# Kernel optimization log

Measured on AMD Instinct MI355X. Metric: run time of the kernel, lower is better.

## Reference

```python
import jax, jax.numpy as jnp
import numpy as np

N = 50000
E = 1600000
NEG_SLOPE = 0.2
BN_EPS = 1e-5


def gat_conv(x, src, dst, W, a_s, a_d, b):
    """PyG-style GATConv (concat=True). a_s/a_d: [H, C]."""
    H, C = a_s.shape
    h = (x @ W).reshape(-1, H, C)  # [N, H, C]
    alpha_src = jnp.einsum('nhc,hc->nh', h, a_s)  # [N, H]
    alpha_dst = jnp.einsum('nhc,hc->nh', h, a_d)  # [N, H]
    e = jax.nn.leaky_relu(alpha_src[src] + alpha_dst[dst], NEG_SLOPE)  # [E, H]
    # segment softmax over edges sharing the same destination node
    m = jax.ops.segment_max(e, dst, num_segments=N)
    e = jnp.exp(e - m[dst])
    s = jax.ops.segment_sum(e, dst, num_segments=N)
    alpha = e / (s[dst] + 1e-16)  # [E, H]
    msg = h[src] * alpha[:, :, None]  # [E, H, C]
    out = jax.ops.segment_sum(msg, dst, num_segments=N)  # [N, H, C]
    return out.reshape(-1, H * C) + b


def batch_norm(x, g, beta):
    mu = jnp.mean(x, axis=0)
    var = jnp.var(x, axis=0)
    return (x - mu) * jax.lax.rsqrt(var + BN_EPS) * g + beta


def setup_inputs() -> dict:
    key = jax.random.key(0)
    ks = jax.random.split(key, 20)
    d_in, hid, heads, d_out = 128, 16, 4, 40
    hh = hid * heads  # 64
    inp = {
        'x': jax.random.normal(ks[0], (N, d_in), jnp.float32),
        'edge_index': jax.random.randint(ks[1], (2, E), 0, N, jnp.int32),
        # layer 0: in -> hid*heads
        'W0': jax.random.normal(ks[2], (d_in, hh), jnp.float32) * 0.05,
        'a_src0': jax.random.normal(ks[3], (heads, hid), jnp.float32) * 0.05,
        'a_dst0': jax.random.normal(ks[4], (heads, hid), jnp.float32) * 0.05,
        'b0': jnp.zeros((hh,), jnp.float32),
        'g0': jnp.ones((hh,), jnp.float32),
        'beta0': jnp.zeros((hh,), jnp.float32),
        # layer 1: hid*heads -> hid*heads
        'W1': jax.random.normal(ks[5], (hh, hh), jnp.float32) * 0.1,
        'a_src1': jax.random.normal(ks[6], (heads, hid), jnp.float32) * 0.1,
        'a_dst1': jax.random.normal(ks[7], (heads, hid), jnp.float32) * 0.1,
        'b1': jnp.zeros((hh,), jnp.float32),
        'g1': jnp.ones((hh,), jnp.float32),
        'beta1': jnp.zeros((hh,), jnp.float32),
        # layer 2: hid*heads -> out, heads=1
        'W2': jax.random.normal(ks[8], (hh, d_out), jnp.float32) * 0.1,
        'a_src2': jax.random.normal(ks[9], (1, d_out), jnp.float32) * 0.1,
        'a_dst2': jax.random.normal(ks[10], (1, d_out), jnp.float32) * 0.1,
        'b2': jnp.zeros((d_out,), jnp.float32),
    }
    return inp


def reference(x, edge_index, W0, a_src0, a_dst0, b0, g0, beta0,
              W1, a_src1, a_dst1, b1, g1, beta1,
              W2, a_src2, a_dst2, b2):
    # add self-loops (PyG GATConv default)
    loop = jnp.arange(N, dtype=edge_index.dtype)
    src = jnp.concatenate([edge_index[0], loop])
    dst = jnp.concatenate([edge_index[1], loop])

    h = gat_conv(x, src, dst, W0, a_src0, a_dst0, b0)
    h = jax.nn.relu(batch_norm(h, g0, beta0))
    h = gat_conv(h, src, dst, W1, a_src1, a_dst1, b1)
    h = jax.nn.relu(batch_norm(h, g1, beta1))
    h = gat_conv(h, src, dst, W2, a_src2, a_dst2, b2)
    return jax.nn.log_softmax(h, axis=-1)
```

## Files before the change

### kernel.cpp

```cpp
#include <hip/hip_runtime.h>
#include <math.h>

#define NEG_SLOPE 0.2f
#define CAP 128
#define BCAP 6144

__device__ __forceinline__ unsigned enc_f(float f) {
    unsigned b = __float_as_uint(f);
    return (b & 0x80000000u) ? ~b : (b | 0x80000000u);
}
__device__ __forceinline__ float dec_f(unsigned u) {
    return (u & 0x80000000u) ? __uint_as_float(u ^ 0x80000000u) : __uint_as_float(~u);
}
#define ENC_NEG_INF 0x007FFFFFu

__device__ __forceinline__ unsigned short f2bf(float f) {
    unsigned u = __float_as_uint(f);
    u += 0x7fffu + ((u >> 16) & 1u);
    return (unsigned short)(u >> 16);
}
__device__ __forceinline__ float bf2f(unsigned short b) {
    return __uint_as_float(((unsigned)b) << 16);
}

static inline int nblk(long total, int b) { return (int)((total + b - 1) / b); }

__global__ void init_kernel(int* bincnt, float* bn, unsigned* menc, int nbin) {
    int i = blockIdx.x * blockDim.x + threadIdx.x;
    if (i < nbin) bincnt[i] = 0;
    if (i < 256) bn[i] = 0.f;
    if (i < 16) menc[i] = ENC_NEG_INF;
}

__global__ void bin_kernel(const int* __restrict__ srcs, const int* __restrict__ dsts,
                           int E_, int EA, int nbin, int* bincnt, unsigned* __restrict__ binbuf) {
    __shared__ int lh[512];
    __shared__ int lbase[512];
    int tid = threadIdx.x;
    for (int i = tid; i < nbin; i += 256) lh[i] = 0;
    __syncthreads();
    int chunk = (EA + gridDim.x - 1) / gridDim.x;
    int e0 = blockIdx.x * chunk;
    int e1 = e0 + chunk; if (e1 > EA) e1 = EA;
    for (int i = e0 + tid; i < e1; i += 256) {
        int d = (i < E_) ? dsts[i] : (i - E_);
        atomicAdd(&lh[d >> 7], 1);
    }
    __syncthreads();
    for (int i = tid; i < nbin; i += 256) {
        lbase[i] = atomicAdd(&bincnt[i], lh[i]);
        lh[i] = 0;
    }
    __syncthreads();
    for (int i = e0 + tid; i < e1; i += 256) {
        int s, d;
        if (i < E_) { s = srcs[i]; d = dsts[i]; } else { s = d = i - E_; }
        int b = d >> 7;
        int pos = lbase[b] + atomicAdd(&lh[b], 1);
        if (pos < BCAP) binbuf[(size_t)b * BCAP + pos] = ((unsigned)s << 16) | (unsigned)d;
    }
}

__global__ void build_kernel(const unsigned* __restrict__ binbuf, const int* __restrict__ bincnt,
                             unsigned short* __restrict__ esrc, int* __restrict__ cnt, int n) {
    __shared__ unsigned short slab[128 * CAP];
    __shared__ int lcnt[128];
    int tid = threadIdx.x;
    int b = blockIdx.x, d0 = b << 7;
    if (tid < 128) lcnt[tid] = 0;
    __syncthreads();
    int nb = bincnt[b]; if (nb > BCAP) nb = BCAP;
    for (int i = tid; i < nb; i += 256) {
        unsigned u = binbuf[(size_t)b * BCAP + i];
        int s = (int)(u >> 16);
        int ld = (int)(u & 0xffffu) - d0;
        int pos = atomicAdd(&lcnt[ld], 1);
        if (pos < CAP) slab[ld * CAP + pos] = (unsigned short)s;
    }
    __syncthreads();
    const uint4* sl = (const uint4*)slab;
    uint4* outp = (uint4*)esrc;
    for (int i = tid; i < 128 * CAP / 8; i += 256) {
        int r = i >> 4;
        if (d0 + r < n) outp[(size_t)(d0 + r) * (CAP / 8) + (i & 15)] = sl[i];
    }
    if (tid < 128 && d0 + tid < n) cnt[d0 + tid] = lcnt[tid];
}

template <int K, bool BN>
__global__ __launch_bounds__(256) void gemm_alpha_kernel(
    const float* __restrict__ X, const float* __restrict__ W,
    const float* __restrict__ a_s, const float* __restrict__ a_d,
    unsigned short* __restrict__ Hout, float* __restrict__ as_o,
    float* __restrict__ ad_o, unsigned* menc_, int n,
    const float* __restrict__ bnsum, const float* __restrict__ bnsq,
    const float* __restrict__ g, const float* __restrict__ beta) {
    __shared__ float Xs[32][132];
    __shared__ float Ws[32][64];
    __shared__ float scale[BN ? K : 4];
    __shared__ float shift[BN ? K : 4];
    __shared__ float redm[4][4];

    int tid = threadIdx.x;
    if (BN) {
        if (tid < K) {
            float inv_n = 1.0f / (float)n;
            float mu = bnsum[tid] * inv_n;
            float var = bnsq[tid] * inv_n - mu * mu;
            float sc = rsqrtf(var + 1e-5f) * g[tid];
            scale[tid] = sc;
            shift[tid] = beta[tid] - mu * sc;
        }
        __syncthreads();
    }

    int node0 = blockIdx.x * 128;
    int tx = tid & 7;
    int ty = tid >> 3;

    int snode = tid & 127;
    int khalf = (tid >> 7) * 16;
    int src_row = node0 + snode; if (src_row >= n) src_row = n - 1;
    const float* xrow = X + (size_t)src_row * K;

    float acc[4][8];
#pragma unroll
    for (int i = 0; i < 4; ++i)
#pragma unroll
        for (int j = 0; j < 8; ++j) acc[i][j] = 0.f;

    constexpr int NCH = K / 32;
    for (int c = 0; c < NCH; ++c) {
        int k0 = c * 32;
#pragma unroll
        for (int r = 0; r < 2; ++r) {
            int f = tid + r * 256;
            int kk = f >> 4;
            int cq = f & 15;
            float4 wv4 = *(const float4*)(W + (size_t)(k0 + kk) * 64 + cq * 4);
            *(float4*)&Ws[kk][cq * 4] = wv4;
        }
#pragma unroll
        for (int q = 0; q < 4; ++q) {
            int kk = khalf + q * 4;
            float4 v = *(const float4*)(xrow + k0 + kk);
            if (BN) {
                float4 sc = *(const float4*)(&scale[k0 + kk]);
                float4 sh = *(const float4*)(&shift[k0 + kk]);
                v.x = fmaxf(fmaf(v.x, sc.x, sh.x), 0.f);
                v.y = fmaxf(fmaf(v.y, sc.y, sh.y), 0.f);
                v.z = fmaxf(fmaf(v.z, sc.z, sh.z), 0.f);
                v.w = fmaxf(fmaf(v.w, sc.w, sh.w), 0.f);
            }
            Xs[kk + 0][snode] = v.x;
            Xs[kk + 1][snode] = v.y;
            Xs[kk + 2][snode] = v.z;
            Xs[kk + 3][snode] = v.w;
        }
        __syncthreads();
#pragma unroll 2
        for (int kk = 0; kk < 32; ++kk) {
            float4 xv = *(const float4*)(&Xs[kk][ty * 4]);
            float4 wa = *(const float4*)(&Ws[kk][tx * 8]);
            float4 wb = *(const float4*)(&Ws[kk][tx * 8 + 4]);
            float xs_[4] = {xv.x, xv.y, xv.z, xv.w};
            float ws_[8] = {wa.x, wa.y, wa.z, wa.w, wb.x, wb.y, wb.z, wb.w};
#pragma unroll
            for (int i = 0; i < 4; ++i)
#pragma unroll
                for (int j = 0; j < 8; ++j)
                    acc[i][j] = fmaf(xs_[i], ws_[j], acc[i][j]);
        }
        __syncthreads();
    }

    float4 asa = *(const float4*)(a_s + tx * 8);
    float4 asb = *(const float4*)(a_s + tx * 8 + 4);
    float4 ada = *(const float4*)(a_d + tx * 8);
    float4 adb = *(const float4*)(a_d + tx * 8 + 4);
    int head = tx >> 1;
    float p1v[4], p2v[4];
#pragma unroll
    for (int i = 0; i < 4; ++i) {
        float p1 = acc[i][0] * asa.x + acc[i][1] * asa.y + acc[i][2] * asa.z + acc[i][3] * asa.w
                 + acc[i][4] * asb.x + acc[i][5] * asb.y + acc[i][6] * asb.z + acc[i][7] * asb.w;
        float p2 = acc[i][0] * ada.x + acc[i][1] * ada.y + acc[i][2] * ada.z + acc[i][3] * ada.w
                 + acc[i][4] * adb.x + acc[i][5] * adb.y + acc[i][6] * adb.z + acc[i][7] * adb.w;
        p1 += __shfl_xor(p1, 1, 64);
        p2 += __shfl_xor(p2, 1, 64);
        p1v[i] = p1; p2v[i] = p2;
    }
#pragma unroll
    for (int i = 0; i < 4; ++i) {
        int node = node0 + ty * 4 + i;
        if (node < n) {
            unsigned r0 = (unsigned)f2bf(acc[i][0]) | ((unsigned)f2bf(acc[i][1]) << 16);
            unsigned r1 = (unsigned)f2bf(acc[i][2]) | ((unsigned)f2bf(acc[i][3]) << 16);
            unsigned r2 = (unsigned)f2bf(acc[i][4]) | ((unsigned)f2bf(acc[i][5]) << 16);
            unsigned r3 = (unsigned)f2bf(acc[i][6]) | ((unsigned)f2bf(acc[i][7]) << 16);
            *(uint4*)(Hout + (size_t)node * 64 + tx * 8) = make_uint4(r0, r1, r2, r3);
            if ((tx & 1) == 0) {
                as_o[(size_t)node * 4 + head] = p1v[i];
                ad_o[(size_t)node * 4 + head] = p2v[i];
            }
        }
    }
    float am = -1e30f;
    if ((tx & 1) == 0)
        am = fmaxf(fmaxf(p1v[0], p1v[1]), fmaxf(p1v[2], p1v[3]));
    am = fmaxf(am, __shfl_xor(am, 8, 64));
    am = fmaxf(am, __shfl_xor(am, 16, 64));
    am = fmaxf(am, __shfl_xor(am, 32, 64));
    int lane = tid & 63;
    if (lane < 8 && (lane & 1) == 0) redm[tid >> 6][lane >> 1] = am;
    __syncthreads();
    if (tid < 4) {
        float m = fmaxf(fmaxf(redm[0][tid], redm[1][tid]), fmaxf(redm[2][tid], redm[3][tid]));
        atomicMax(&menc_[tid], enc_f(m));
    }
}

__global__ void gather64_kernel(const int* __restrict__ cnt,
                                const unsigned short* __restrict__ esrc,
                                const float* __restrict__ as_, const float* __restrict__ ad_,
                                const unsigned short* __restrict__ Hf,
                                const unsigned* __restrict__ menc,
                                const float* __restrict__ bias, float* __restrict__ feat, int n) {
    int tid = threadIdx.x;
    int wv = tid >> 6, lane = tid & 63;
    int slot = lane >> 4, ql = lane & 15, hq = ql >> 2;
    int node = blockIdx.x * 4 + wv;
    if (node >= n) return;

    int deg = cnt[node]; if (deg > CAP) deg = CAP;
    const unsigned short* ep = esrc + (size_t)node * CAP;
    float4 adv = *(const float4*)(ad_ + (size_t)node * 4);
    float adh = (slot == 0) ? adv.x : (slot == 1) ? adv.y : (slot == 2) ? adv.z : adv.w;
    float mm = dec_f(menc[slot]) + adh;
    float mh = mm > 0.f ? mm : NEG_SLOPE * mm;

    float4 acc = make_float4(0.f, 0.f, 0.f, 0.f);
    float wp = 0.f;
    int nch = (deg + 15) >> 4;

    int lim0 = deg < 16 ? deg : 16;
    int s0 = (ql < lim0) ? (int)ep[ql] : 0;
    float aA = as_[(unsigned)(s0 * 4 + slot)];
    int sA = 0;
    if (nch > 1) {
        int l1 = deg - 16; if (l1 > 16) l1 = 16;
        sA = (ql < l1) ? (int)ep[16 + ql] : 0;
    }
    ushort4 hva[4], hvb[4];
#pragma unroll
    for (int i = 0; i < 4; ++i) {
        if (i * 4 >= lim0) break;
        int sj = __shfl(s0, i * 4 + slot, 64);
        hva[i] = *(const ushort4*)(Hf + (unsigned)(sj * 64 + ql * 4));
    }
    int sB = 0; float aB = 0.f;

#define G64_CHUNK(c, hC, hN, sC, sN, aC, aN)                                      \
    {                                                                             \
        int lim = deg - (c) * 16; if (lim > 16) lim = 16;                         \
        float ev = aC + adh;                                                      \
        ev = ev > 0.f ? ev : NEG_SLOPE * ev;                                      \
        float w = (ql < lim) ? __expf(ev - mh) : 0.f;                             \
        if ((c) + 1 < nch) aN = as_[(unsigned)(sC * 4 + slot)];                   \
        if ((c) + 2 < nch) {                                                      \
            int l2 = deg - ((c) + 2) * 16; if (l2 > 16) l2 = 16;                  \
            sN = (ql < l2) ? (int)ep[((c) + 2) * 16 + ql] : 0;                    \
        }                                                                         \
        if ((c) + 1 < nch) {                                                      \
            int limN = deg - ((c) + 1) * 16; if (limN > 16) limN = 16;            \
            _Pragma("unroll")                                                     \
            for (int i = 0; i < 4; ++i) {                                         \
                if (i * 4 >= limN) break;                                         \
                int sj = __shfl(sC, i * 4 + slot, 64);                            \
                hN[i] = *(const ushort4*)(Hf + (unsigned)(sj * 64 + ql * 4));     \
            }                                                                     \
        }                                                                         \
        wp += w;                                                                  \
        _Pragma("unroll")                                                         \
        for (int i = 0; i < 4; ++i) {                                             \
            if (i * 4 >= lim) break;                                              \
            int cj = i * 4 + slot;                                                \
            float wj = __shfl(w, hq * 16 + cj, 64);                               \
            ushort4 hv = hC[i];                                                   \
            acc.x = fmaf(bf2f(hv.x), wj, acc.x);                                  \
            acc.y = fmaf(bf2f(hv.y), wj, acc.y);                                  \
            acc.z = fmaf(bf2f(hv.z), wj, acc.z);                                  \
            acc.w = fmaf(bf2f(hv.w), wj, acc.w);                                  \
        }                                                                         \
    }

    for (int c = 0; c < nch; c += 2) {
        G64_CHUNK(c, hva, hvb, sA, sB, aA, aB);
        if (c + 1 < nch) G64_CHUNK(c + 1, hvb, hva, sB, sA, aB, aA);
    }
#undef G64_CHUNK

#pragma unroll
    for (int o = 16; o < 64; o <<= 1) {
        acc.x += __shfl_xor(acc.x, o, 64);
        acc.y += __shfl_xor(acc.y, o, 64);
        acc.z += __shfl_xor(acc.z, o, 64);
        acc.w += __shfl_xor(acc.w, o, 64);
    }
#pragma unroll
    for (int o = 1; o < 16; o <<= 1) wp += __shfl_xor(wp, o, 64);
    float wsh = __shfl(wp, hq << 4, 64);
    if (slot == 0) {
        float inv = 1.0f / (wsh + 1e-16f);
        float4 bv = *(const float4*)(bias + ql * 4);
        float4 rr;
        rr.x = fmaf(acc.x, inv, bv.x);
        rr.y = fmaf(acc.y, inv, bv.y);
        rr.z = fmaf(acc.z, inv, bv.z);
        rr.w = fmaf(acc.w, inv, bv.w);
        *(float4*)(feat + (size_t)node * 64 + ql * 4) = rr;
    }
}

__global__ void prep2_kernel(const float* __restrict__ feat, const float* __restrict__ bnsum,
                             const float* __restrict__ bnsq, const float* __restrict__ g,
                             const float* __restrict__ beta, const float* __restrict__ W2,
                             const float* __restrict__ as2v, const float* __restrict__ ad2v,
                             unsigned short* __restrict__ z, float* __restrict__ as_o,
                             float* __restrict__ ad_o, unsigned* menc_, int n) {
    __shared__ float sc[64], sh[64], vs[64], vd[64];
    int tid = threadIdx.x;
    if (tid < 64) {
        float inv_n = 1.0f / (float)n;
        float mu = bnsum[tid] * inv_n;
        float var = bnsq[tid] * inv_n - mu * mu;
        float s = rsqrtf(var + 1e-5f) * g[tid];
        sc[tid] = s;
        sh[tid] = beta[tid] - mu * s;
    } else if (tid < 128) {
        int k = tid - 64;
        float s1 = 0.f, s2 = 0.f;
        for (int j = 0; j < 40; ++j) {
            float wv = W2[k * 40 + j];
            s1 = fmaf(wv, as2v[j], s1);
            s2 = fmaf(wv, ad2v[j], s2);
        }
        vs[k] = s1;
        vd[k] = s2;
    }
    __syncthreads();
    int lane = tid & 63, wv = tid >> 6;
    float scl = sc[lane], shl = sh[lane], vsl = vs[lane], vdl = vd[lane];
    float amax = -1e30f;
    int nwaves = gridDim.x * 4;
    for (int node = blockIdx.x * 4 + wv; node < n; node += nwaves) {
        float v = fmaf(feat[(size_t)node * 64 + lane], scl, shl);
        v = v > 0.f ? v : 0.f;
        z[(size_t)node * 64 + lane] = f2bf(v);
        float p1 = v * vsl, p2 = v * vdl;
#pragma unroll
        for (int o = 1; o < 64; o <<= 1) {
            p1 += __shfl_xor(p1, o, 64);
            p2 += __shfl_xor(p2, o, 64);
        }
        amax = fmaxf(amax, p1);
        if (lane == 0) { as_o[node] = p1; ad_o[node] = p2; }
    }
    if (lane == 0) atomicMax(menc_, enc_f(amax));
}

__global__ void gatherz_kernel(const int* __restrict__ cnt,
                               const unsigned short* __restrict__ esrc,
                               const float* __restrict__ as_, const float* __restrict__ ad_,
                               const unsigned short* __restrict__ Z,
                               const unsigned* __restrict__ menc,
                               float* __restrict__ agg, int n) {
    int tid = threadIdx.x;
    int wv = tid >> 6, lane = tid & 63;
    int slot = lane >> 4, ql = lane & 15;
    int node = blockIdx.x * 4 + wv;
    if (node >= n) return;

    int deg = cnt[node]; if (deg > CAP) deg = CAP;
    const unsigned short* ep = esrc + (size_t)node * CAP;
    float adv = ad_[node];
    float mm = dec_f(menc[0]) + adv;
    float mh = mm > 0.f ? mm : NEG_SLOPE * mm;

    float4 acc = make_float4(0.f, 0.f, 0.f, 0.f);
    float wp = 0.f;
    for (int base = 0; base < deg; base += 64) {
        int lim = deg - base; if (lim > 64) lim = 64;
        int s = 0;
        if (lane < lim) s = (int)ep[base + lane];
        float asv = (lane < lim) ? as_[(unsigned)s] : 0.f;
        ushort4 hv[16];
#pragma unroll
        for (int i = 0; i < 16; ++i) {
            if (i * 4 >= lim) break;
            int sj = __shfl(s, i * 4 + slot, 64);
            hv[i] = *(const ushort4*)(Z + (unsigned)(sj * 64 + ql * 4));
        }
        float w = 0.f;
        if (lane < lim) {
            float ev = asv + adv;
            ev = ev > 0.f ? ev : NEG_SLOPE * ev;
            w = __expf(ev - mh);
        }
        wp += w;
#pragma unroll
        for (int i = 0; i < 16; ++i) {
            if (i * 4 >= lim) break;
            int cj = i * 4 + slot;
            float wj = __shfl(w, cj, 64);
            ushort4 h4 = hv[i];
            acc.x = fmaf(bf2f(h4.x), wj, acc.x);
            acc.y = fmaf(bf2f(h4.y), wj, acc.y);
            acc.z = fmaf(bf2f(h4.z), wj, acc.z);
            acc.w = fmaf(bf2f(h4.w), wj, acc.w);
        }
    }
#pragma unroll
    for (int o = 16; o < 64; o <<= 1) {
        acc.x += __shfl_xor(acc.x, o, 64);
        acc.y += __shfl_xor(acc.y, o, 64);
        acc.z += __shfl_xor(acc.z, o, 64);
        acc.w += __shfl_xor(acc.w, o, 64);
    }
#pragma unroll
    for (int o = 1; o < 64; o <<= 1) wp += __shfl_xor(wp, o, 64);
    if (slot == 0) {
        float inv = 1.0f / (wp + 1e-16f);
        float4 rr;
        rr.x = acc.x * inv;
        rr.y = acc.y * inv;
        rr.z = acc.z * inv;
        rr.w = acc.w * inv;
        *(float4*)(agg + (size_t)node * 64 + ql * 4) = rr;
    }
}

__global__ __launch_bounds__(256) void gemm_lsm_kernel(const float* __restrict__ X,
                                                       const float* __restrict__ W,
                                                       const float* __restrict__ bias,
                                                       float* __restrict__ out, int n) {
    __shared__ float Xs[32][132];
    __shared__ float Ws[32][40];
    __shared__ float bs[40];
    int tid = threadIdx.x;
    if (tid < 40) bs[tid] = bias[tid];

    int node0 = blockIdx.x * 128;
    int tx = tid & 7;
    int ty = tid >> 3;
    int snode = tid & 127;
    int khalf = (tid >> 7) * 16;
    int src_row = node0 + snode; if (src_row >= n) src_row = n - 1;
    const float* xrow = X + (size_t)src_row * 64;

    float acc[4][5];
#pragma unroll
    for (int i = 0; i < 4; ++i)
#pragma unroll
        for (int j = 0; j < 5; ++j) acc[i][j] = 0.f;

    for (int c = 0; c < 2; ++c) {
        int k0 = c * 32;
        for (int f = tid; f < 320; f += 256) {
            int kk = f / 10, q = f - kk * 10;
            *(float4*)&Ws[kk][q * 4] = *(const float4*)(W + (size_t)(k0 + kk) * 40 + q * 4);
        }
#pragma unroll
        for (int q = 0; q < 4; ++q) {
            int kk = khalf + q * 4;
            float4 v = *(const float4*)(xrow + k0 + kk);
            Xs[kk + 0][snode] = v.x;
            Xs[kk + 1][snode] = v.y;
            Xs[kk + 2][snode] = v.z;
            Xs[kk + 3][snode] = v.w;
        }
        __syncthreads();
#pragma unroll 2
        for (int kk = 0; kk < 32; ++kk) {
            float4 xv = *(const float4*)(&Xs[kk][ty * 4]);
            float w0 = Ws[kk][tx * 5 + 0];
            float w1 = Ws[kk][tx * 5 + 1];
            float w2 = Ws[kk][tx * 5 + 2];
            float w3 = Ws[kk][tx * 5 + 3];
            float w4 = Ws[kk][tx * 5 + 4];
            float xs_[4] = {xv.x, xv.y, xv.z, xv.w};
#pragma unroll
            for (int i = 0; i < 4; ++i) {
                acc[i][0] = fmaf(xs_[i], w0, acc[i][0]);
                acc[i][1] = fmaf(xs_[i], w1, acc[i][1]);
                acc[i][2] = fmaf(xs_[i], w2, acc[i][2]);
                acc[i][3] = fmaf(xs_[i], w3, acc[i][3]);
                acc[i][4] = fmaf(xs_[i], w4, acc[i][4]);
            }
        }
        __syncthreads();
    }

    float b0 = bs[tx * 5 + 0], b1 = bs[tx * 5 + 1], b2 = bs[tx * 5 + 2],
          b3 = bs[tx * 5 + 3], b4 = bs[tx * 5 + 4];
#pragma unroll
    for (int i = 0; i < 4; ++i) {
        float v0 = acc[i][0] + b0, v1 = acc[i][1] + b1, v2 = acc[i][2] + b2,
              v3 = acc[i][3] + b3, v4 = acc[i][4] + b4;
        float m = fmaxf(fmaxf(fmaxf(v0, v1), fmaxf(v2, v3)), v4);
        m = fmaxf(m, __shfl_xor(m, 1, 64));
        m = fmaxf(m, __shfl_xor(m, 2, 64));
        m = fmaxf(m, __shfl_xor(m, 4, 64));
        float ex = __expf(v0 - m) + __expf(v1 - m) + __expf(v2 - m)
                 + __expf(v3 - m) + __expf(v4 - m);
        ex += __shfl_xor(ex, 1, 64);
        ex += __shfl_xor(ex, 2, 64);
        ex += __shfl_xor(ex, 4, 64);
        float ls = m + logf(ex);
        int node = node0 + ty * 4 + i;
        if (node < n) {
            float* op = out + (size_t)node * 40 + tx * 5;
            op[0] = v0 - ls;
            op[1] = v1 - ls;
            op[2] = v2 - ls;
            op[3] = v3 - ls;
            op[4] = v4 - ls;
        }
    }
}

__global__ void bn_stats_kernel(const float* __restrict__ feat, float* bnsum, float* bnsq,
                                int n) {
    __shared__ float ls[256], lq[256];
    int f = threadIdx.x & 63, y = threadIdx.x >> 6;
    float ps = 0.f, pq = 0.f;
    for (int node = blockIdx.x * 4 + y; node < n; node += gridDim.x * 4) {
        float v = feat[(size_t)node * 64 + f];
        ps += v;
        pq += v * v;
    }
    ls[threadIdx.x] = ps;
    lq[threadIdx.x] = pq;
    __syncthreads();
    if (y == 0) {
        atomicAdd(&bnsum[f], ls[f] + ls[f + 64] + ls[f + 128] + ls[f + 192]);
        atomicAdd(&bnsq[f], lq[f] + lq[f + 64] + lq[f + 128] + lq[f + 192]);
    }
}

extern "C" void kernel_launch(void* const* d_in, const int* in_sizes, int n_in,
                              void* d_out, int out_size, void* d_ws, size_t ws_size,
                              hipStream_t stream) {
    const float* x   = (const float*)d_in[0];
    const int*   ei  = (const int*)d_in[1];
    const float* W0  = (const float*)d_in[2];
    const float* as0 = (const float*)d_in[3];
    const float* ad0 = (const float*)d_in[4];
    const float* b0  = (const float*)d_in[5];
    const float* g0  = (const float*)d_in[6];
    const float* be0 = (const float*)d_in[7];
    const float* W1  = (const float*)d_in[8];
    const float* as1 = (const float*)d_in[9];
    const float* ad1 = (const float*)d_in[10];
    const float* b1  = (const float*)d_in[11];
    const float* g1  = (const float*)d_in[12];
    const float* be1 = (const float*)d_in[13];
    const float* W2  = (const float*)d_in[14];
    const float* as2 = (const float*)d_in[15];
    const float* ad2 = (const float*)d_in[16];
    const float* b2  = (const float*)d_in[17];

    const int N  = in_sizes[0] / 128;
    const int E  = in_sizes[1] / 2;
    const int EA = E + N;
    const int NBIN = (N + 127) >> 7;
    const int* srcs = ei;
    const int* dsts = ei + E;

    float* ws    = (float*)d_ws;
    float* feat  = ws;
    float* agg   = feat + (size_t)N * 64;
    float* asrc  = agg + (size_t)N * 64;
    float* adst  = asrc + (size_t)N * 4;
    float* bn    = adst + (size_t)N * 4;
    unsigned* menc = (unsigned*)(bn + 256);
    int* bincnt  = (int*)(menc + 16);
    int* cnt     = bincnt + 512;
    unsigned short* hb   = (unsigned short*)(cnt + N);
    unsigned short* esrc = hb + (size_t)N * 64;
    unsigned* binbuf = (unsigned*)(esrc + (size_t)N * CAP);

    float* bn0sum = bn, *bn0sq = bn + 64, *bn1sum = bn + 128, *bn1sq = bn + 192;

    init_kernel<<<2, 256, 0, stream>>>(bincnt, bn, menc, NBIN);
    bin_kernel<<<512, 256, 0, stream>>>(srcs, dsts, E, EA, NBIN, bincnt, binbuf);
    build_kernel<<<NBIN, 256, 0, stream>>>(binbuf, bincnt, esrc, cnt, N);

    gemm_alpha_kernel<128, false><<<nblk(N, 128), 256, 0, stream>>>(
        x, W0, as0, ad0, hb, asrc, adst, menc, N, nullptr, nullptr, nullptr, nullptr);
    gather64_kernel<<<nblk(N, 4), 256, 0, stream>>>(cnt, esrc, asrc, adst, hb, menc, b0, feat, N);
    bn_stats_kernel<<<512, 256, 0, stream>>>(feat, bn0sum, bn0sq, N);

    gemm_alpha_kernel<64, true><<<nblk(N, 128), 256, 0, stream>>>(
        feat, W1, as1, ad1, hb, asrc, adst, menc + 4, N, bn0sum, bn0sq, g0, be0);
    gather64_kernel<<<nblk(N, 4), 256, 0, stream>>>(cnt, esrc, asrc, adst, hb, menc + 4, b1,
                                                    feat, N);
    bn_stats_kernel<<<512, 256, 0, stream>>>(feat, bn1sum, bn1sq, N);

    prep2_kernel<<<512, 256, 0, stream>>>(feat, bn1sum, bn1sq, g1, be1, W2, as2, ad2,
                                          hb, asrc, adst, menc + 8, N);
    gatherz_kernel<<<nblk(N, 4), 256, 0, stream>>>(cnt, esrc, asrc, adst, hb, menc + 8, agg, N);
    gemm_lsm_kernel<<<nblk(N, 128), 256, 0, stream>>>(agg, W2, b2, (float*)d_out, N);
}
```

Baseline: 368.3 us.

## Deepen gather prefetch to three-stage rotating buffers in 64-wide GAT aggregation

Changes the per-node edge aggregation loop from double-buffered to triple-buffered prefetch, so neighbor feature rows are loaded two chunks ahead instead of one. It also drops the per-iteration early-break guards in the gather and FMA loops, loading padded entries from index 0 and multiplying them by zero weights. The aim is to hide more gather latency. The cost is more registers, which may lower occupancy, and some wasted loads on partial chunks.

```diff
diff --git a/kernel.cpp b/kernel.cpp
--- a/kernel.cpp
+++ b/kernel.cpp
@@ -243,62 +243,73 @@
     float wp = 0.f;
     int nch = (deg + 15) >> 4;
 
-    int lim0 = deg < 16 ? deg : 16;
-    int s0 = (ql < lim0) ? (int)ep[ql] : 0;
-    float aA = as_[(unsigned)(s0 * 4 + slot)];
+    ushort4 h0[4], h1[4], h2[4];
+    int l0 = deg < 16 ? deg : 16;
+    int sP0 = (ql < l0) ? (int)ep[ql] : 0;
+    float aA = as_[(unsigned)(sP0 * 4 + slot)];
     int sA = 0;
     if (nch > 1) {
         int l1 = deg - 16; if (l1 > 16) l1 = 16;
         sA = (ql < l1) ? (int)ep[16 + ql] : 0;
     }
-    ushort4 hva[4], hvb[4];
+    int sB = 0;
+    if (nch > 2) {
+        int l2 = deg - 32; if (l2 > 16) l2 = 16;
+        sB = (ql < l2) ? (int)ep[32 + ql] : 0;
+    }
 #pragma unroll
     for (int i = 0; i < 4; ++i) {
-        if (i * 4 >= lim0) break;
-        int sj = __shfl(s0, i * 4 + slot, 64);
-        hva[i] = *(const ushort4*)(Hf + (unsigned)(sj * 64 + ql * 4));
-    }
-    int sB = 0; float aB = 0.f;
-
-#define G64_CHUNK(c, hC, hN, sC, sN, aC, aN)                                      \
-    {                                                                             \
-        int lim = deg - (c) * 16; if (lim > 16) lim = 16;                         \
-        float ev = aC + adh;                                                      \
-        ev = ev > 0.f ? ev : NEG_SLOPE * ev;                                      \
-        float w = (ql < lim) ? __expf(ev - mh) : 0.f;                             \
-        if ((c) + 1 < nch) aN = as_[(unsigned)(sC * 4 + slot)];                   \
-        if ((c) + 2 < nch) {                                                      \
-            int l2 = deg - ((c) + 2) * 16; if (l2 > 16) l2 = 16;                  \
-            sN = (ql < l2) ? (int)ep[((c) + 2) * 16 + ql] : 0;                    \
-        }                                                                         \
-        if ((c) + 1 < nch) {                                                      \
-            int limN = deg - ((c) + 1) * 16; if (limN > 16) limN = 16;            \
-            _Pragma("unroll")                                                     \
-            for (int i = 0; i < 4; ++i) {                                         \
-                if (i * 4 >= limN) break;                                         \
-                int sj = __shfl(sC, i * 4 + slot, 64);                            \
-                hN[i] = *(const ushort4*)(Hf + (unsigned)(sj * 64 + ql * 4));     \
-            }                                                                     \
-        }                                                                         \
-        wp += w;                                                                  \
-        _Pragma("unroll")                                                         \
-        for (int i = 0; i < 4; ++i) {                                             \
-            if (i * 4 >= lim) break;                                              \
-            int cj = i * 4 + slot;                                                \
-            float wj = __shfl(w, hq * 16 + cj, 64);                               \
-            ushort4 hv = hC[i];                                                   \
-            acc.x = fmaf(bf2f(hv.x), wj, acc.x);                                  \
-            acc.y = fmaf(bf2f(hv.y), wj, acc.y);                                  \
-            acc.z = fmaf(bf2f(hv.z), wj, acc.z);                                  \
-            acc.w = fmaf(bf2f(hv.w), wj, acc.w);                                  \
-        }                                                                         \
-    }
-
-    for (int c = 0; c < nch; c += 2) {
-        G64_CHUNK(c, hva, hvb, sA, sB, aA, aB);
-        if (c + 1 < nch) G64_CHUNK(c + 1, hvb, hva, sB, sA, aB, aA);
-    }
-#undef G64_CHUNK
+        int sj = __shfl(sP0, i * 4 + slot, 64);
+        h0[i] = *(const ushort4*)(Hf + (unsigned)(sj * 64 + ql * 4));
+    }
+    float aB = 0.f;
+    if (nch > 1) {
+        aB = as_[(unsigned)(sA * 4 + slot)];
+#pragma unroll
+        for (int i = 0; i < 4; ++i) {
+            int sj = __shfl(sA, i * 4 + slot, 64);
+            h1[i] = *(const ushort4*)(Hf + (unsigned)(sj * 64 + ql * 4));
+        }
+    }
+    float aC = 0.f;
+    int sC = 0;
+
+#define GBODY(cc, HC, HD, S2, S3, AC, A2)                                     \
+    {                                                                         \
+        int lim = deg - (cc) * 16; if (lim > 16) lim = 16;                    \
+        float ev = AC + adh;                                                  \
+        ev = ev > 0.f ? ev : NEG_SLOPE * ev;                                  \
+        float w = (ql < lim) ? __expf(ev - mh) : 0.f;                         \
+        if ((cc) + 2 < nch) A2 = as_[(unsigned)(S2 * 4 + slot)];              \
+        if ((cc) + 3 < nch) {                                                 \
+            int l3 = deg - ((cc) + 3) * 16; if (l3 > 16) l3 = 16;             \
+            S3 = (ql < l3) ? (int)ep[((cc) + 3) * 16 + ql] : 0;               \
+        }                                                                     \
+        if ((cc) + 2 < nch) {                                                 \
+            _Pragma("unroll")                                                 \
+            for (int i = 0; i < 4; ++i) {                                     \
+                int sj = __shfl(S2, i * 4 + slot, 64);                        \
+                HD[i] = *(const ushort4*)(Hf + (unsigned)(sj * 64 + ql * 4)); \
+            }                                                                 \
+        }                                                                     \
+        wp += w;                                                              \
+        _Pragma("unroll")                                                     \
+        for (int i = 0; i < 4; ++i) {                                         \
+            float wj = __shfl(w, hq * 16 + i * 4 + slot, 64);                 \
+            ushort4 hv = HC[i];                                               \
+            acc.x = fmaf(bf2f(hv.x), wj, acc.x);                              \
+            acc.y = fmaf(bf2f(hv.y), wj, acc.y);                              \
+            acc.z = fmaf(bf2f(hv.z), wj, acc.z);                              \
+            acc.w = fmaf(bf2f(hv.w), wj, acc.w);                              \
+        }                                                                     \
+    }
+
+    for (int c = 0; c < nch; c += 3) {
+        GBODY(c, h0, h2, sB, sC, aA, aC);
+        if (c + 1 < nch) GBODY(c + 1, h1, h0, sC, sA, aB, aA);
+        if (c + 2 < nch) GBODY(c + 2, h2, h1, sA, sB, aC, aB);
+    }
+#undef GBODY
 
 #pragma unroll
     for (int o = 16; o < 64; o <<= 1) {
```

After: 372.4 us. Within noise of the previous version (+1.1%).

## Sort destination nodes by degree to balance gather wavefront work

Applied to the files above, without the earlier changes.

Adds a degree histogram, prefix scan and scatter pass that builds a permutation of nodes ordered by descending in-degree. The three gather kernels now process nodes through this permutation, so the four waves in a block get similar edge counts and the heaviest nodes are scheduled first. The aim is less divergence and tail imbalance within blocks. The cost is three extra small launches, one indirection per wave, and the loss of node locality in the feature writes and ad_ reads.

```diff
diff --git a/kernel.cpp b/kernel.cpp
--- a/kernel.cpp
+++ b/kernel.cpp
@@ -25,11 +25,12 @@
 
 static inline int nblk(long total, int b) { return (int)((total + b - 1) / b); }
 
-__global__ void init_kernel(int* bincnt, float* bn, unsigned* menc, int nbin) {
+__global__ void init_kernel(int* bincnt, float* bn, unsigned* menc, int* degbin, int nbin) {
     int i = blockIdx.x * blockDim.x + threadIdx.x;
     if (i < nbin) bincnt[i] = 0;
     if (i < 256) bn[i] = 0.f;
     if (i < 16) menc[i] = ENC_NEG_INF;
+    if (i < 132) degbin[i] = 0;
 }
 
 __global__ void bin_kernel(const int* __restrict__ srcs, const int* __restrict__ dsts,
@@ -85,6 +86,34 @@
         if (d0 + r < n) outp[(size_t)(d0 + r) * (CAP / 8) + (i & 15)] = sl[i];
     }
     if (tid < 128 && d0 + tid < n) cnt[d0 + tid] = lcnt[tid];
+}
+
+__global__ void hist_kernel(const int* __restrict__ cnt, int* degbin, int n) {
+    int i = blockIdx.x * 256 + threadIdx.x;
+    if (i < n) {
+        int d = cnt[i]; if (d > CAP) d = CAP;
+        atomicAdd(&degbin[CAP - d], 1);
+    }
+}
+__global__ void scan_kernel(int* degbin) {
+    __shared__ int sb[CAP + 1];
+    int t = threadIdx.x;
+    if (t < CAP + 1) sb[t] = degbin[t];
+    __syncthreads();
+    if (t == 0) {
+        int acc = 0;
+        for (int i = 0; i < CAP + 1; ++i) { int v = sb[i]; sb[i] = acc; acc += v; }
+    }
+    __syncthreads();
+    if (t < CAP + 1) degbin[t] = sb[t];
+}
+__global__ void scatter_kernel(const int* __restrict__ cnt, int* degbin, int* perm, int n) {
+    int i = blockIdx.x * 256 + threadIdx.x;
+    if (i < n) {
+        int d = cnt[i]; if (d > CAP) d = CAP;
+        int pos = atomicAdd(&degbin[CAP - d], 1);
+        perm[pos] = i;
+    }
 }
 
 template <int K, bool BN>
@@ -220,7 +249,7 @@
     }
 }
 
-__global__ void gather64_kernel(const int* __restrict__ cnt,
+__global__ void gather64_kernel(const int* __restrict__ perm, const int* __restrict__ cnt,
                                 const unsigned short* __restrict__ esrc,
                                 const float* __restrict__ as_, const float* __restrict__ ad_,
                                 const unsigned short* __restrict__ Hf,
@@ -229,8 +258,9 @@
     int tid = threadIdx.x;
     int wv = tid >> 6, lane = tid & 63;
     int slot = lane >> 4, ql = lane & 15, hq = ql >> 2;
-    int node = blockIdx.x * 4 + wv;
-    if (node >= n) return;
+    int gid = blockIdx.x * 4 + wv;
+    if (gid >= n) return;
+    int node = perm[gid];
 
     int deg = cnt[node]; if (deg > CAP) deg = CAP;
     const unsigned short* ep = esrc + (size_t)node * CAP;
@@ -369,7 +399,7 @@
     if (lane == 0) atomicMax(menc_, enc_f(amax));
 }
 
-__global__ void gatherz_kernel(const int* __restrict__ cnt,
+__global__ void gatherz_kernel(const int* __restrict__ perm, const int* __restrict__ cnt,
                                const unsigned short* __restrict__ esrc,
                                const float* __restrict__ as_, const float* __restrict__ ad_,
                                const unsigned short* __restrict__ Z,
@@ -378,8 +408,9 @@
     int tid = threadIdx.x;
     int wv = tid >> 6, lane = tid & 63;
     int slot = lane >> 4, ql = lane & 15;
-    int node = blockIdx.x * 4 + wv;
-    if (node >= n) return;
+    int gid = blockIdx.x * 4 + wv;
+    if (gid >= n) return;
+    int node = perm[gid];
 
     int deg = cnt[node]; if (deg > CAP) deg = CAP;
     const unsigned short* ep = esrc + (size_t)node * CAP;
@@ -589,26 +620,33 @@
     unsigned short* hb   = (unsigned short*)(cnt + N);
     unsigned short* esrc = hb + (size_t)N * 64;
     unsigned* binbuf = (unsigned*)(esrc + (size_t)N * CAP);
+    int* degbin = (int*)(binbuf + (size_t)NBIN * BCAP);
+    int* perm   = degbin + 132;
 
     float* bn0sum = bn, *bn0sq = bn + 64, *bn1sum = bn + 128, *bn1sq = bn + 192;
 
-    init_kernel<<<2, 256, 0, stream>>>(bincnt, bn, menc, NBIN);
+    init_kernel<<<2, 256, 0, stream>>>(bincnt, bn, menc, degbin, NBIN);
     bin_kernel<<<512, 256, 0, stream>>>(srcs, dsts, E, EA, NBIN, bincnt, binbuf);
     build_kernel<<<NBIN, 256, 0, stream>>>(binbuf, bincnt, esrc, cnt, N);
+    hist_kernel<<<nblk(N, 256), 256, 0, stream>>>(cnt, degbin, N);
+    scan_kernel<<<1, 256, 0, stream>>>(degbin);
+    scatter_kernel<<<nblk(N, 256), 256, 0, stream>>>(cnt, degbin, perm, N);
 
     gemm_alpha_kernel<128, false><<<nblk(N, 128), 256, 0, stream>>>(
         x, W0, as0, ad0, hb, asrc, adst, menc, N, nullptr, nullptr, nullptr, nullptr);
-    gather64_kernel<<<nblk(N, 4), 256, 0, stream>>>(cnt, esrc, asrc, adst, hb, menc, b0, feat, N);
+    gather64_kernel<<<nblk(N, 4), 256, 0, stream>>>(perm, cnt, esrc, asrc, adst, hb, menc, b0,
+                                                    feat, N);
     bn_stats_kernel<<<512, 256, 0, stream>>>(feat, bn0sum, bn0sq, N);
 
     gemm_alpha_kernel<64, true><<<nblk(N, 128), 256, 0, stream>>>(
         feat, W1, as1, ad1, hb, asrc, adst, menc + 4, N, bn0sum, bn0sq, g0, be0);
-    gather64_kernel<<<nblk(N, 4), 256, 0, stream>>>(cnt, esrc, asrc, adst, hb, menc + 4, b1,
-                                                    feat, N);
+    gather64_kernel<<<nblk(N, 4), 256, 0, stream>>>(perm, cnt, esrc, asrc, adst, hb, menc + 4,
+                                                    b1, feat, N);
     bn_stats_kernel<<<512, 256, 0, stream>>>(feat, bn1sum, bn1sq, N);
 
     prep2_kernel<<<512, 256, 0, stream>>>(feat, bn1sum, bn1sq, g1, be1, W2, as2, ad2,
                                           hb, asrc, adst, menc + 8, N);
-    gatherz_kernel<<<nblk(N, 4), 256, 0, stream>>>(cnt, esrc, asrc, adst, hb, menc + 8, agg, N);
+    gatherz_kernel<<<nblk(N, 4), 256, 0, stream>>>(perm, cnt, esrc, asrc, adst, hb, menc + 8,
+                                                   agg, N);
     gemm_lsm_kernel<<<nblk(N, 128), 256, 0, stream>>>(agg, W2, b2, (float*)d_out, N);
 }
```

New measurement: 560.0 us. 52.1% more time.
